# Optimization experiments

Hardware: AMD Instinct MI355X
Metric: run time of the kernel (lower is better)

The kernel has to match this reference:

```python
import jax, jax.numpy as jnp
import numpy as np


def setup_inputs() -> dict:
    key = jax.random.key(0)
    k1, k2 = jax.random.split(key)
    B, N, M = 8, 4096, 4096
    points1 = jax.random.normal(k1, (B, N, 3), dtype=jnp.float32)
    points2 = jax.random.normal(k2, (B, M, 3), dtype=jnp.float32)
    return {"points1": points1, "points2": points2}


def reference(points1, points2):
    x2 = jnp.sum(points1 * points1, axis=-1)            # [B, N]
    y2 = jnp.sum(points2 * points2, axis=-1)            # [B, M]
    xy = jnp.einsum('bnd,bmd->bnm', points1, points2)   # [B, N, M]
    d = x2[:, :, None] + y2[:, None, :] - 2.0 * xy      # [B, N, M]
    dist1 = jnp.min(d, axis=2)                          # [B, N] NN dist p1->p2
    dist2 = jnp.min(d, axis=1)                          # [B, M] NN dist p2->p1
    # Symmetric Hausdorff: max over each direction, then max of the two, sum over batch
    m = jnp.maximum(jnp.max(dist1, axis=-1), jnp.max(dist2, axis=-1))  # [B]
    return jnp.sum(m)
```

## Files before the change

### kernel.cpp

```cpp
#include <hip/hip_runtime.h>
#include <float.h>

#define B_CONST 8
#define GROUPS 16
#define QSPLIT 8

typedef float v2f __attribute__((ext_vector_type(2)));

__global__ void hd_pack(const float* __restrict__ p1, const float* __restrict__ p2,
                        float* __restrict__ o1, float* __restrict__ o2,
                        unsigned int* __restrict__ comm, int n1, int n2) {
    int i = blockIdx.x * blockDim.x + threadIdx.x;
    if (blockIdx.x == 0 && threadIdx.x < 9) comm[threadIdx.x] = 0u;
    const float* src; float* dst; int idx;
    if (i < n1)           { src = p1; dst = o1; idx = i; }
    else if (i < n1 + n2) { src = p2; dst = o2; idx = i - n1; }
    else return;
    size_t s = 3 * (size_t)idx;
    float x = src[s], y = src[s + 1], z = src[s + 2];
    float w = fmaf(x, x, fmaf(y, y, z * z));
    float* base = dst + (size_t)(idx >> 1) * 8 + (idx & 1);
    base[0] = -2.0f * x; base[2] = -2.0f * y; base[4] = -2.0f * z; base[6] = w;
}

__global__ __launch_bounds__(256) void hd_nnmax(
    const float* __restrict__ p1raw, const float* __restrict__ p2raw,
    const float* __restrict__ pk1, const float* __restrict__ pk2,
    float* __restrict__ part, int N, int M, int blocksDir0) {
    int blk = blockIdx.x;
    const float* qraw; const float* rpk; int QN, RM, dir;
    if (blk < blocksDir0) { qraw = p1raw; rpk = pk2; QN = N; RM = M; dir = 0; }
    else { blk -= blocksDir0; qraw = p2raw; rpk = pk1; QN = M; RM = N; dir = 1; }

    int qblocks = QN >> 9;
    int perB = qblocks * GROUPS;
    int b    = blk / perB;
    int rem  = blk - b * perB;
    int qblk = rem / GROUPS;
    int g    = rem - qblk * GROUPS;

    int l = threadIdx.x & 63;
    int w = __builtin_amdgcn_readfirstlane((int)(threadIdx.x >> 6));

    const float* qb = qraw + 3 * ((size_t)b * QN + ((size_t)qblk << 9));
    v2f QX[8], QY[8], QZ[8], MN[8];
    #pragma unroll
    for (int s = 0; s < 8; ++s) {
        int q = s * 64 + l;
        float x = qb[3 * q], y = qb[3 * q + 1], z = qb[3 * q + 2];
        QX[s] = (v2f){ x, x };
        QY[s] = (v2f){ y, y };
        QZ[s] = (v2f){ z, z };
        MN[s] = (v2f){ FLT_MAX, FLT_MAX };
    }

    int cnt = RM / (2 * GROUPS * 4);
    const v2f* rb = (const v2f*)rpk +
        ((size_t)b * (RM >> 1) + (size_t)(g * 4 + w) * cnt) * 4;

    #pragma unroll 4
    for (int j = 0; j < cnt; ++j) {
        v2f RX = rb[4 * j + 0];
        v2f RY = rb[4 * j + 1];
        v2f RZ = rb[4 * j + 2];
        v2f RW = rb[4 * j + 3];
        #pragma unroll
        for (int s = 0; s < 8; ++s) {
            v2f a = __builtin_elementwise_fma(QX[s], RX, RW);
            a = __builtin_elementwise_fma(QY[s], RY, a);
            a = __builtin_elementwise_fma(QZ[s], RZ, a);
            MN[s] = __builtin_elementwise_min(MN[s], a);
        }
    }

    __shared__ float red[2048];
    #pragma unroll
    for (int s = 0; s < 8; ++s)
        red[(w << 9) + s * 64 + l] = fminf(MN[s].x, MN[s].y);
    __syncthreads();

    size_t dirOff = dir ? (size_t)GROUPS * B_CONST * N : 0;
    float* pb = part + dirOff + ((size_t)g * B_CONST + b) * QN + ((size_t)qblk << 9);
    for (int t = threadIdx.x; t < 512; t += 256) {
        float m = fminf(fminf(red[t], red[512 + t]),
                        fminf(red[1024 + t], red[1536 + t]));
        float x = qb[3 * t], y = qb[3 * t + 1], z = qb[3 * t + 2];
        float w2 = fmaf(x, x, fmaf(y, y, z * z));
        pb[t] = fmaxf(w2 + m, 0.0f);
    }
}

__global__ __launch_bounds__(256) void hd_final(
    const float* __restrict__ part, unsigned int* __restrict__ comm,
    float* __restrict__ out, int N, int M) {
    int db  = blockIdx.x >> 3;
    int qs  = blockIdx.x & (QSPLIT - 1);
    int dir = db >> 3;
    int b   = db & 7;
    int QN  = dir ? M : N;
    size_t dirOff = dir ? (size_t)GROUPS * B_CONST * N : 0;
    const float* fb = part + dirOff + (size_t)b * QN;
    size_t gs = (size_t)B_CONST * QN;

    int span = QN / QSPLIT;
    int q0 = qs * span;
    float mx = 0.0f;
    for (int qq = q0 + threadIdx.x; qq < q0 + span; qq += 256) {
        float mm = fb[qq];
        #pragma unroll
        for (int gg = 1; gg < GROUPS; ++gg)
            mm = fminf(mm, fb[(size_t)gg * gs + qq]);
        mx = fmaxf(mx, mm);
    }
    #pragma unroll
    for (int off = 32; off > 0; off >>= 1)
        mx = fmaxf(mx, __shfl_down(mx, off, 64));
    __shared__ float wred[4];
    int l = threadIdx.x & 63, w = threadIdx.x >> 6;
    if (l == 0) wred[w] = mx;
    __syncthreads();
    if (threadIdx.x == 0) {
        mx = fmaxf(fmaxf(wred[0], wred[1]), fmaxf(wred[2], wred[3]));
        atomicMax(&comm[b], __float_as_uint(mx));
        __threadfence();
        unsigned int t2 = atomicAdd(&comm[8], 1u);
        if (t2 == (unsigned int)(16 * QSPLIT - 1)) {
            float s = 0.0f;
            for (int bb = 0; bb < B_CONST; ++bb)
                s += __uint_as_float(atomicMax(&comm[bb], 0u));
            out[0] = s;
        }
    }
}

extern "C" void kernel_launch(void* const* d_in, const int* in_sizes, int n_in,
                              void* d_out, int out_size, void* d_ws, size_t ws_size,
                              hipStream_t stream) {
    const float* p1 = (const float*)d_in[0];
    const float* p2 = (const float*)d_in[1];
    const int B = B_CONST;
    int N = in_sizes[0] / (3 * B);
    int M = in_sizes[1] / (3 * B);
    int n1 = B * N, n2 = B * M;

    char* ws = (char*)d_ws;
    float* pk1 = (float*)ws;
    float* pk2 = (float*)(ws + (size_t)n1 * 4 * sizeof(float));
    float* part = (float*)(ws + (size_t)(n1 + n2) * 4 * sizeof(float));
    unsigned int* comm = (unsigned int*)(part + (size_t)GROUPS * (n1 + n2));

    int packBlocks = (n1 + n2 + 255) / 256;
    hd_pack<<<packBlocks, 256, 0, stream>>>(p1, p2, pk1, pk2, comm, n1, n2);

    int blocksDir0 = B * (N >> 9) * GROUPS;
    int blocksDir1 = B * (M >> 9) * GROUPS;
    hd_nnmax<<<blocksDir0 + blocksDir1, 256, 0, stream>>>(
        p1, p2, pk1, pk2, part, N, M, blocksDir0);

    hd_final<<<16 * QSPLIT, 256, 0, stream>>>(part, comm, (float*)d_out, N, M);
}
```

Baseline: 83.39 us.

## Fuse reference packing into NN kernel via LDS staging and halve group count

Drops the separate pack kernel. Each NN block now loads its slice of raw reference points, converts them to the scaled layout (-2x, -2y, -2z, |r|^2) in shared memory, and reads them from LDS in the inner loop. The query squared norms are also cached in shared memory, and the comm reset moves into the main kernel. GROUPS drops from 16 to 8, so each block covers 512 references, the grid is halved and the partial buffer shrinks. This removes one launch and a global round trip for the packed data, but adds per-block staging and extra syncs, and the grid has fewer blocks.

```diff
diff --git a/kernel.cpp b/kernel.cpp
--- a/kernel.cpp
+++ b/kernel.cpp
@@ -2,35 +2,21 @@
 #include <float.h>
 
 #define B_CONST 8
-#define GROUPS 16
+#define GROUPS 8
 #define QSPLIT 8
 
 typedef float v2f __attribute__((ext_vector_type(2)));
 
-__global__ void hd_pack(const float* __restrict__ p1, const float* __restrict__ p2,
-                        float* __restrict__ o1, float* __restrict__ o2,
-                        unsigned int* __restrict__ comm, int n1, int n2) {
-    int i = blockIdx.x * blockDim.x + threadIdx.x;
-    if (blockIdx.x == 0 && threadIdx.x < 9) comm[threadIdx.x] = 0u;
-    const float* src; float* dst; int idx;
-    if (i < n1)           { src = p1; dst = o1; idx = i; }
-    else if (i < n1 + n2) { src = p2; dst = o2; idx = i - n1; }
-    else return;
-    size_t s = 3 * (size_t)idx;
-    float x = src[s], y = src[s + 1], z = src[s + 2];
-    float w = fmaf(x, x, fmaf(y, y, z * z));
-    float* base = dst + (size_t)(idx >> 1) * 8 + (idx & 1);
-    base[0] = -2.0f * x; base[2] = -2.0f * y; base[4] = -2.0f * z; base[6] = w;
-}
-
 __global__ __launch_bounds__(256) void hd_nnmax(
     const float* __restrict__ p1raw, const float* __restrict__ p2raw,
-    const float* __restrict__ pk1, const float* __restrict__ pk2,
-    float* __restrict__ part, int N, int M, int blocksDir0) {
+    float* __restrict__ part, unsigned int* __restrict__ comm,
+    int N, int M, int blocksDir0) {
     int blk = blockIdx.x;
-    const float* qraw; const float* rpk; int QN, RM, dir;
-    if (blk < blocksDir0) { qraw = p1raw; rpk = pk2; QN = N; RM = M; dir = 0; }
-    else { blk -= blocksDir0; qraw = p2raw; rpk = pk1; QN = M; RM = N; dir = 1; }
+    if (blk == 0 && threadIdx.x < 9) comm[threadIdx.x] = 0u;
+
+    const float* qraw; const float* rraw; int QN, RM, dir;
+    if (blk < blocksDir0) { qraw = p1raw; rraw = p2raw; QN = N; RM = M; dir = 0; }
+    else { blk -= blocksDir0; qraw = p2raw; rraw = p1raw; QN = M; RM = N; dir = 1; }
 
     int qblocks = QN >> 9;
     int perB = qblocks * GROUPS;
@@ -42,28 +28,44 @@
     int l = threadIdx.x & 63;
     int w = __builtin_amdgcn_readfirstlane((int)(threadIdx.x >> 6));
 
+    __shared__ float buf[2048];
+    __shared__ float qw_s[512];
+
+    int refsPerGroup = RM / GROUPS;
+    const float* rsrc = rraw + 3 * ((size_t)b * RM + (size_t)g * refsPerGroup);
+    {
+        int i = threadIdx.x;
+        float x0 = rsrc[6*i],   y0 = rsrc[6*i+1], z0 = rsrc[6*i+2];
+        float x1 = rsrc[6*i+3], y1 = rsrc[6*i+4], z1 = rsrc[6*i+5];
+        float* t = buf + 8 * i;
+        t[0] = -2.0f * x0; t[1] = -2.0f * x1;
+        t[2] = -2.0f * y0; t[3] = -2.0f * y1;
+        t[4] = -2.0f * z0; t[5] = -2.0f * z1;
+        t[6] = fmaf(x0, x0, fmaf(y0, y0, z0 * z0));
+        t[7] = fmaf(x1, x1, fmaf(y1, y1, z1 * z1));
+    }
+
     const float* qb = qraw + 3 * ((size_t)b * QN + ((size_t)qblk << 9));
     v2f QX[8], QY[8], QZ[8], MN[8];
     #pragma unroll
     for (int s = 0; s < 8; ++s) {
         int q = s * 64 + l;
-        float x = qb[3 * q], y = qb[3 * q + 1], z = qb[3 * q + 2];
+        float x = qb[3*q], y = qb[3*q+1], z = qb[3*q+2];
         QX[s] = (v2f){ x, x };
         QY[s] = (v2f){ y, y };
         QZ[s] = (v2f){ z, z };
         MN[s] = (v2f){ FLT_MAX, FLT_MAX };
+        if (w == 0) qw_s[q] = fmaf(x, x, fmaf(y, y, z * z));
     }
+    __syncthreads();
 
-    int cnt = RM / (2 * GROUPS * 4);
-    const v2f* rb = (const v2f*)rpk +
-        ((size_t)b * (RM >> 1) + (size_t)(g * 4 + w) * cnt) * 4;
-
+    const v2f* lp = (const v2f*)buf + (size_t)(w * 64) * 4;
     #pragma unroll 4
-    for (int j = 0; j < cnt; ++j) {
-        v2f RX = rb[4 * j + 0];
-        v2f RY = rb[4 * j + 1];
-        v2f RZ = rb[4 * j + 2];
-        v2f RW = rb[4 * j + 3];
+    for (int j = 0; j < 64; ++j) {
+        v2f RX = lp[4*j + 0];
+        v2f RY = lp[4*j + 1];
+        v2f RZ = lp[4*j + 2];
+        v2f RW = lp[4*j + 3];
         #pragma unroll
         for (int s = 0; s < 8; ++s) {
             v2f a = __builtin_elementwise_fma(QX[s], RX, RW);
@@ -72,21 +74,19 @@
             MN[s] = __builtin_elementwise_min(MN[s], a);
         }
     }
+    __syncthreads();
 
-    __shared__ float red[2048];
     #pragma unroll
     for (int s = 0; s < 8; ++s)
-        red[(w << 9) + s * 64 + l] = fminf(MN[s].x, MN[s].y);
+        buf[(w << 9) + s * 64 + l] = fminf(MN[s].x, MN[s].y);
     __syncthreads();
 
     size_t dirOff = dir ? (size_t)GROUPS * B_CONST * N : 0;
     float* pb = part + dirOff + ((size_t)g * B_CONST + b) * QN + ((size_t)qblk << 9);
     for (int t = threadIdx.x; t < 512; t += 256) {
-        float m = fminf(fminf(red[t], red[512 + t]),
-                        fminf(red[1024 + t], red[1536 + t]));
-        float x = qb[3 * t], y = qb[3 * t + 1], z = qb[3 * t + 2];
-        float w2 = fmaf(x, x, fmaf(y, y, z * z));
-        pb[t] = fmaxf(w2 + m, 0.0f);
+        float m = fminf(fminf(buf[t], buf[512 + t]),
+                        fminf(buf[1024 + t], buf[1536 + t]));
+        pb[t] = fmaxf(qw_s[t] + m, 0.0f);
     }
 }
 
@@ -144,18 +144,13 @@
     int n1 = B * N, n2 = B * M;
 
     char* ws = (char*)d_ws;
-    float* pk1 = (float*)ws;
-    float* pk2 = (float*)(ws + (size_t)n1 * 4 * sizeof(float));
-    float* part = (float*)(ws + (size_t)(n1 + n2) * 4 * sizeof(float));
+    float* part = (float*)ws;
     unsigned int* comm = (unsigned int*)(part + (size_t)GROUPS * (n1 + n2));
-
-    int packBlocks = (n1 + n2 + 255) / 256;
-    hd_pack<<<packBlocks, 256, 0, stream>>>(p1, p2, pk1, pk2, comm, n1, n2);
 
     int blocksDir0 = B * (N >> 9) * GROUPS;
     int blocksDir1 = B * (M >> 9) * GROUPS;
     hd_nnmax<<<blocksDir0 + blocksDir1, 256, 0, stream>>>(
-        p1, p2, pk1, pk2, part, N, M, blocksDir0);
+        p1, p2, part, comm, N, M, blocksDir0);
 
     hd_final<<<16 * QSPLIT, 256, 0, stream>>>(part, comm, (float*)d_out, N, M);
 }
```

Result: no change. 82.62 us (-0.9%).
